# Kernel tuning notes

Measured on AMD Instinct MI355X. Metric: run time of the kernel, lower is better.

## Reference

```python
import jax, jax.numpy as jnp
import numpy as np

B, T = 512, 256
DX, DZ, DH, DDZ, DDX = 1024, 256, 512, 256, 256


def setup_inputs() -> dict:
    key = jax.random.key(0)
    ks = jax.random.split(key, 16)
    s = 0.05
    return {
        "eps": jax.random.normal(ks[0], (B, T, DZ), jnp.float32),
        # stoch_trans dz: h -> relu -> (loc, softplus scale)
        "dz_W1": jax.random.normal(ks[1], (DDZ, DH), jnp.float32) * s,
        "dz_b1": jnp.zeros((DDZ,), jnp.float32),
        "dz_Wloc": jax.random.normal(ks[2], (DZ, DDZ), jnp.float32) * s,
        "dz_bloc": jnp.zeros((DZ,), jnp.float32),
        "dz_Wscale": jax.random.normal(ks[3], (DZ, DDZ), jnp.float32) * s,
        "dz_bscale": jnp.zeros((DZ,), jnp.float32),
        # GRU cell (PyTorch layout: gates [r, z, n] stacked)
        "gru_Wih": jax.random.normal(ks[4], (3 * DH, DZ), jnp.float32) * s,
        "gru_Whh": jax.random.normal(ks[5], (3 * DH, DH), jnp.float32) * s,
        "gru_bih": jnp.zeros((3 * DH,), jnp.float32),
        "gru_bhh": jnp.zeros((3 * DH,), jnp.float32),
        # emitter dx: h -> relu -> sigmoid probs
        "dx_W1": jax.random.normal(ks[6], (DDX, DH), jnp.float32) * s,
        "dx_b1": jnp.zeros((DDX,), jnp.float32),
        "dx_W2": jax.random.normal(ks[7], (DX, DDX), jnp.float32) * s,
        "dx_b2": jnp.zeros((DX,), jnp.float32),
        "h0": jnp.zeros((DH,), jnp.float32),
    }


def reference(eps, dz_W1, dz_b1, dz_Wloc, dz_bloc, dz_Wscale, dz_bscale,
              gru_Wih, gru_Whh, gru_bih, gru_bhh,
              dx_W1, dx_b1, dx_W2, dx_b2, h0):
    batch = eps.shape[0]
    h_init = jnp.broadcast_to(h0[None, :], (batch, h0.shape[0]))

    def step(h, eps_t):
        # stochastic transition: z_loc, z_scale from h_{t-1}
        hid = jax.nn.relu(h @ dz_W1.T + dz_b1)
        z_loc = hid @ dz_Wloc.T + dz_bloc
        z_scale = jax.nn.softplus(hid @ dz_Wscale.T + dz_bscale)
        z_t = z_loc + z_scale * eps_t  # reparameterized Normal sample
        # GRU cell (torch equations)
        gi = z_t @ gru_Wih.T + gru_bih
        gh = h @ gru_Whh.T + gru_bhh
        i_r, i_z, i_n = jnp.split(gi, 3, axis=-1)
        h_r, h_z, h_n = jnp.split(gh, 3, axis=-1)
        r = jax.nn.sigmoid(i_r + h_r)
        u = jax.nn.sigmoid(i_z + h_z)
        n = jnp.tanh(i_n + r * h_n)
        h_new = (1.0 - u) * n + u * h
        # emitter: Bernoulli probs
        hid2 = jax.nn.relu(h_new @ dx_W1.T + dx_b1)
        x_ps = jax.nn.sigmoid(hid2 @ dx_W2.T + dx_b2)
        return h_new, x_ps

    eps_tb = jnp.swapaxes(eps, 0, 1)  # [T, B, DZ]
    _, x_ps = jax.lax.scan(step, h_init, eps_tb)
    return jnp.swapaxes(x_ps, 0, 1)  # [B, T, DX]
```

## Files before the change

kernel.cpp:

```cpp
#include <hip/hip_runtime.h>
#include <hip/hip_bf16.h>

#define DEV __device__ __forceinline__

typedef __bf16 bf16x8 __attribute__((ext_vector_type(8)));
typedef float  f32x4  __attribute__((ext_vector_type(4)));

constexpr int BB  = 512;
constexpr int TT  = 256;
constexpr int DX  = 1024;
constexpr int DZ  = 256;
constexpr int DH  = 512;

DEV f32x4 mfma16(bf16x8 a, bf16x8 b, f32x4 c) {
    return __builtin_amdgcn_mfma_f32_16x16x32_bf16(a, b, c, 0, 0, 0);
}
DEV float sigf(float x) { return 1.0f / (1.0f + __expf(-x)); }
DEV float tanhf_(float x) {
    float e = __expf(-2.0f * fabsf(x));
    float r = (1.0f - e) / (1.0f + e);
    return copysignf(r, x);
}
DEV float softplusf(float x) {
    float m = fmaxf(x, 0.0f);
    return m + __logf(__expf(x - m) + __expf(-m));
}

DEV void st16_wt(void* p, bf16x8 v) {
    asm volatile("global_store_dwordx4 %0, %1, off sc0 sc1" :: "v"(p), "v"(v) : "memory");
}
DEV void st_flag(unsigned* p, unsigned v) {
    asm volatile("global_store_dword %0, %1, off sc0 sc1" :: "v"(p), "v"(v) : "memory");
}
DEV unsigned ld_flag(const unsigned* p) {
    unsigned v;
    asm volatile("global_load_dword %0, %1, off sc0 sc1\n\ts_waitcnt vmcnt(0)"
                 : "=v"(v) : "v"(p) : "memory");
    return v;
}
#define CC_LOAD(dst, p) \
    asm volatile("global_load_dwordx4 %0, %1, off sc0 sc1" : "=v"(dst) : "v"(p))
#define VMCNT0 do { \
    asm volatile("s_waitcnt vmcnt(0)" ::: "memory"); \
    __builtin_amdgcn_sched_barrier(0); } while (0)
#define LGKM0 do { \
    asm volatile("s_waitcnt lgkmcnt(0)" ::: "memory"); \
    __builtin_amdgcn_sched_barrier(0); } while (0)

DEV void wave_wait(const unsigned* base, int nslots, int wv, unsigned tgt) {
    const int lane = threadIdx.x & 63;
    const unsigned* p = base + (((lane & (nslots - 1)) * 4 + wv) * 32);
    while (true) {
        unsigned v = ld_flag(p);
        if (__all((int)(v >= tgt))) break;
    }
}

struct CvtArgs {
    const float* src[7];
    __bf16* dst[7];
    int n[7];
};
__global__ void cvt_weights(CvtArgs a, const float* h0, __bf16* h0buf) {
    int idx = blockIdx.x * blockDim.x + threadIdx.x;
    int stride = gridDim.x * blockDim.x;
    for (int s = 0; s < 7; ++s) {
        const float* sp = a.src[s];
        __bf16* dp = a.dst[s];
        int n = a.n[s];
        for (int i = idx; i < n; i += stride) dp[i] = (__bf16)sp[i];
    }
    for (int i = idx; i < 512 * 512; i += stride) h0buf[i] = (__bf16)h0[i & 511];
}

__global__ __launch_bounds__(256, 1) void phase1c(
    const float* __restrict__ eps,
    const float* __restrict__ b1,  const float* __restrict__ bloc,
    const float* __restrict__ bscale, const float* __restrict__ bih,
    const float* __restrict__ bhh,
    const __bf16* __restrict__ wW1,   const __bf16* __restrict__ wWloc,
    const __bf16* __restrict__ wWscale, const __bf16* __restrict__ wWih,
    const __bf16* __restrict__ wWhh,
    const __bf16* __restrict__ h0buf,
    unsigned* __restrict__ flags,
    char* __restrict__ outb)
{
    __shared__ __bf16 lds[75776];

    const int tid  = threadIdx.x;
    const int w    = tid >> 6;
    const int lane = tid & 63;
    const int r16  = lane & 15;
    const int g4   = lane >> 4;
    const int g    = blockIdx.x & 7;
    const int r    = blockIdx.x >> 3;
    unsigned* gfl   = flags + g * 4096;
    unsigned* flagA = gfl;
    unsigned* flagB = gfl + 2048;
    unsigned* flagC = gfl + 3072;
    const int rowW  = g * 64 + w * 16;

    auto stage = [&](const __bf16* src, __bf16* dst, int R, int C) {
        int chunks = R * C / 8;
        for (int ch = tid; ch < chunks; ch += 256) {
            int row = ch / (C / 8), cc = (ch % (C / 8)) * 8;
            bf16x8 v = *(const bf16x8*)(src + (size_t)row * C + cc);
            *(bf16x8*)(dst + ((row * C + cc) ^ ((row & 7) << 3))) = v;
        }
    };

    if (r < 8) {
        stage(wW1     + (size_t)(r * 32) * 512, lds,         32, 512);
        stage(wWloc   + (size_t)(r * 32) * 256, lds + 16384, 32, 256);
        stage(wWscale + (size_t)(r * 32) * 256, lds + 24576, 32, 256);
        __bf16* wb = lds + 32768 + w * 512;
        const int zc0 = r * 32;
        float bb1[2], bbl[2], bbs[2];
        #pragma unroll
        for (int tt = 0; tt < 2; ++tt) {
            int c = zc0 + tt * 16 + r16;
            bb1[tt] = b1[c]; bbl[tt] = bloc[c]; bbs[tt] = bscale[c];
        }
        __syncthreads();

        for (int t = 0; t < TT; ++t) {
            float ev[2][4];
            #pragma unroll
            for (int tt = 0; tt < 2; ++tt)
                #pragma unroll
                for (int i = 0; i < 4; ++i) {
                    int row = rowW + 4 * g4 + i;
                    ev[tt][i] = __builtin_nontemporal_load(
                        eps + ((size_t)row * TT + t) * DZ + zc0 + tt * 16 + r16);
                }
            if (t) wave_wait(flagA, 16, w, t);
            const char* hp = (t == 0)
                ? (const char*)(h0buf + (size_t)(rowW + r16) * 512) + g4 * 16
                : outb + ((size_t)(rowW + r16) * TT + (t - 1)) * 4096 + 2048 + g4 * 16;
            bf16x8 hv[16];
            #pragma unroll
            for (int kk = 0; kk < 16; ++kk) CC_LOAD(hv[kk], hp + kk * 64);
            VMCNT0;
            f32x4 acc0 = {0,0,0,0}, acc1 = {0,0,0,0};
            #pragma unroll
            for (int kk = 0; kk < 16; ++kk) {
                int l0 = r16, l1 = 16 + r16;
                acc0 = mfma16(hv[kk], *(const bf16x8*)(lds + ((l0 * 512 + kk * 32 + g4 * 8) ^ ((l0 & 7) << 3))), acc0);
                acc1 = mfma16(hv[kk], *(const bf16x8*)(lds + ((l1 * 512 + kk * 32 + g4 * 8) ^ ((l1 & 7) << 3))), acc1);
            }
            #pragma unroll
            for (int tt = 0; tt < 2; ++tt) {
                f32x4 ac = tt ? acc1 : acc0;
                #pragma unroll
                for (int i = 0; i < 4; ++i)
                    wb[(4 * g4 + i) * 32 + tt * 16 + r16] = (__bf16)fmaxf(ac[i] + bb1[tt], 0.0f);
            }
            LGKM0;
            {
                int rl = lane >> 2, ch = lane & 3;
                bf16x8 v = *(const bf16x8*)(wb + rl * 32 + ch * 8);
                st16_wt(outb + ((size_t)(rowW + rl) * TT + t) * 4096 + 3072 + (zc0 + ch * 8) * 2, v);
            }
            VMCNT0;
            if (lane == 0) st_flag(flagB + (r * 4 + w) * 32, t + 1);
            wave_wait(flagB, 8, w, t + 1);
            const char* qp = outb + ((size_t)(rowW + r16) * TT + t) * 4096 + 3072 + g4 * 16;
            bf16x8 qv[8];
            #pragma unroll
            for (int kk = 0; kk < 8; ++kk) CC_LOAD(qv[kk], qp + kk * 64);
            VMCNT0;
            f32x4 aL0 = {0,0,0,0}, aL1 = {0,0,0,0}, aS0 = {0,0,0,0}, aS1 = {0,0,0,0};
            #pragma unroll
            for (int kk = 0; kk < 8; ++kk) {
                int l0 = r16, l1 = 16 + r16;
                int s0 = (l0 * 256 + kk * 32 + g4 * 8) ^ ((l0 & 7) << 3);
                int s1 = (l1 * 256 + kk * 32 + g4 * 8) ^ ((l1 & 7) << 3);
                aL0 = mfma16(qv[kk], *(const bf16x8*)(lds + 16384 + s0), aL0);
                aL1 = mfma16(qv[kk], *(const bf16x8*)(lds + 16384 + s1), aL1);
                aS0 = mfma16(qv[kk], *(const bf16x8*)(lds + 24576 + s0), aS0);
                aS1 = mfma16(qv[kk], *(const bf16x8*)(lds + 24576 + s1), aS1);
            }
            #pragma unroll
            for (int tt = 0; tt < 2; ++tt) {
                f32x4 L = tt ? aL1 : aL0, S = tt ? aS1 : aS0;
                #pragma unroll
                for (int i = 0; i < 4; ++i) {
                    float z = (L[i] + bbl[tt]) + softplusf(S[i] + bbs[tt]) * ev[tt][i];
                    wb[(4 * g4 + i) * 32 + tt * 16 + r16] = (__bf16)z;
                }
            }
            LGKM0;
            {
                int rl = lane >> 2, ch = lane & 3;
                bf16x8 v = *(const bf16x8*)(wb + rl * 32 + ch * 8);
                st16_wt(outb + ((size_t)(rowW + rl) * TT + t) * 4096 + 3584 + (zc0 + ch * 8) * 2, v);
            }
            VMCNT0;
            if (lane == 0) st_flag(flagC + (r * 4 + w) * 32, t + 1);
        }
    } else {
        const int c0 = (r - 8) * 32;
        for (int gg = 0; gg < 3; ++gg) {
            stage(wWhh + (size_t)(512 * gg + c0) * 512, lds + gg * 16384, 32, 512);
            stage(wWih + (size_t)(512 * gg + c0) * 256, lds + 49152 + gg * 8192, 32, 256);
        }
        __bf16* wb = lds + 73728 + w * 512;
        float bI[3][2], bH[3][2];
        #pragma unroll
        for (int gg = 0; gg < 3; ++gg)
            #pragma unroll
            for (int tt = 0; tt < 2; ++tt) {
                int col = 512 * gg + c0 + tt * 16 + r16;
                bI[gg][tt] = bih[col];
                bH[gg][tt] = bhh[col];
            }
        float hreg[2][4];
        #pragma unroll
        for (int tt = 0; tt < 2; ++tt) {
            float v = (float)h0buf[c0 + tt * 16 + r16];
            #pragma unroll
            for (int i = 0; i < 4; ++i) hreg[tt][i] = v;
        }
        __syncthreads();

        for (int t = 0; t < TT; ++t) {
            if (t) wave_wait(flagA, 16, w, t);
            const char* hp = (t == 0)
                ? (const char*)(h0buf + (size_t)(rowW + r16) * 512) + g4 * 16
                : outb + ((size_t)(rowW + r16) * TT + (t - 1)) * 4096 + 2048 + g4 * 16;
            bf16x8 hv[16];
            #pragma unroll
            for (int kk = 0; kk < 16; ++kk) CC_LOAD(hv[kk], hp + kk * 64);
            VMCNT0;
            f32x4 gh[6];
            #pragma unroll
            for (int j = 0; j < 6; ++j) gh[j] = (f32x4){0,0,0,0};
            #pragma unroll
            for (int kk = 0; kk < 16; ++kk) {
                #pragma unroll
                for (int j = 0; j < 6; ++j) {
                    int gg = j >> 1, lr = (j & 1) * 16 + r16;
                    gh[j] = mfma16(hv[kk], *(const bf16x8*)(lds + gg * 16384 +
                              ((lr * 512 + kk * 32 + g4 * 8) ^ ((lr & 7) << 3))), gh[j]);
                }
            }
            wave_wait(flagC, 8, w, t + 1);
            const char* zp = outb + ((size_t)(rowW + r16) * TT + t) * 4096 + 3584 + g4 * 16;
            bf16x8 zv[8];
            #pragma unroll
            for (int kk = 0; kk < 8; ++kk) CC_LOAD(zv[kk], zp + kk * 64);
            VMCNT0;
            f32x4 gi[6];
            #pragma unroll
            for (int j = 0; j < 6; ++j) gi[j] = (f32x4){0,0,0,0};
            #pragma unroll
            for (int kk = 0; kk < 8; ++kk) {
                #pragma unroll
                for (int j = 0; j < 6; ++j) {
                    int gg = j >> 1, lr = (j & 1) * 16 + r16;
                    gi[j] = mfma16(zv[kk], *(const bf16x8*)(lds + 49152 + gg * 8192 +
                              ((lr * 256 + kk * 32 + g4 * 8) ^ ((lr & 7) << 3))), gi[j]);
                }
            }
            #pragma unroll
            for (int tt = 0; tt < 2; ++tt) {
                #pragma unroll
                for (int i = 0; i < 4; ++i) {
                    float rr = sigf(gi[0 + tt][i] + bI[0][tt] + gh[0 + tt][i] + bH[0][tt]);
                    float uu = sigf(gi[2 + tt][i] + bI[1][tt] + gh[2 + tt][i] + bH[1][tt]);
                    float nn = tanhf_(gi[4 + tt][i] + bI[2][tt] + rr * (gh[4 + tt][i] + bH[2][tt]));
                    float hv2 = (1.0f - uu) * nn + uu * hreg[tt][i];
                    hreg[tt][i] = hv2;
                    wb[(4 * g4 + i) * 32 + tt * 16 + r16] = (__bf16)hv2;
                }
            }
            LGKM0;
            {
                int rl = lane >> 2, ch = lane & 3;
                bf16x8 v = *(const bf16x8*)(wb + rl * 32 + ch * 8);
                st16_wt(outb + ((size_t)(rowW + rl) * TT + t) * 4096 + 2048 + (c0 + ch * 8) * 2, v);
            }
            VMCNT0;
            if (lane == 0) st_flag(flagA + ((r - 8) * 4 + w) * 32, t + 1);
        }
    }
}

__global__ __launch_bounds__(256, 3) void phase2(
    const float* __restrict__ db1, const float* __restrict__ db2,
    const __bf16* __restrict__ W1, const __bf16* __restrict__ W2,
    float* __restrict__ out)
{
    __shared__ __bf16 hS  [32 * 512];
    __shared__ __bf16 hid2[32 * 256];

    const int tid  = threadIdx.x;
    const int w    = tid >> 6;
    const int lane = tid & 63;
    const int r16  = lane & 15;
    const int g4   = lane >> 4;
    const size_t row0 = (size_t)blockIdx.x * 32;

    #pragma unroll
    for (int it = 0; it < 8; ++it) {
        int chunk = it * 256 + tid;
        int row = chunk >> 6;
        int cc  = (chunk & 63) * 8;
        bf16x8 v = __builtin_nontemporal_load(
            (const bf16x8*)((const char*)out + (row0 + row) * 4096 + 2048 + cc * 2));
        *(bf16x8*)(hS + ((row * 512 + cc) ^ ((row & 7) << 3))) = v;
    }
    __syncthreads();

    {
        f32x4 acc[2][4];
        #pragma unroll
        for (int rt = 0; rt < 2; ++rt)
            #pragma unroll
            for (int ct = 0; ct < 4; ++ct) acc[rt][ct] = (f32x4){0,0,0,0};
        const __bf16* pB[4];
        #pragma unroll
        for (int ct = 0; ct < 4; ++ct)
            pB[ct] = W1 + (w * 64 + 16 * ct + r16) * 512 + g4 * 8;
        #pragma unroll
        for (int kk = 0; kk < 16; ++kk) {
            bf16x8 a[2];
            #pragma unroll
            for (int rt = 0; rt < 2; ++rt) {
                int row = rt * 16 + r16;
                a[rt] = *(const bf16x8*)(hS + ((row * 512 + kk * 32 + g4 * 8) ^ ((row & 7) << 3)));
            }
            #pragma unroll
            for (int ct = 0; ct < 4; ++ct) {
                bf16x8 b = *(const bf16x8*)(pB[ct] + kk * 32);
                acc[0][ct] = mfma16(a[0], b, acc[0][ct]);
                acc[1][ct] = mfma16(a[1], b, acc[1][ct]);
            }
        }
        #pragma unroll
        for (int ct = 0; ct < 4; ++ct) {
            int col = w * 64 + 16 * ct + r16;
            float bias = db1[col];
            #pragma unroll
            for (int rt = 0; rt < 2; ++rt)
                #pragma unroll
                for (int i = 0; i < 4; ++i) {
                    int row = rt * 16 + g4 * 4 + i;
                    hid2[(row * 256 + col) ^ ((row & 7) << 3)] =
                        (__bf16)fmaxf(acc[rt][ct][i] + bias, 0.0f);
                }
        }
    }
    __syncthreads();

    #pragma unroll
    for (int c = 0; c < 4; ++c) {
        f32x4 acc[2][4];
        #pragma unroll
        for (int rt = 0; rt < 2; ++rt)
            #pragma unroll
            for (int ct = 0; ct < 4; ++ct) acc[rt][ct] = (f32x4){0,0,0,0};
        const __bf16* pB[4];
        #pragma unroll
        for (int ct = 0; ct < 4; ++ct)
            pB[ct] = W2 + (w * 256 + c * 64 + 16 * ct + r16) * 256 + g4 * 8;
        #pragma unroll
        for (int kk = 0; kk < 8; ++kk) {
            bf16x8 a[2];
            #pragma unroll
            for (int rt = 0; rt < 2; ++rt) {
                int row = rt * 16 + r16;
                a[rt] = *(const bf16x8*)(hid2 + ((row * 256 + kk * 32 + g4 * 8) ^ ((row & 7) << 3)));
            }
            #pragma unroll
            for (int ct = 0; ct < 4; ++ct) {
                bf16x8 b = *(const bf16x8*)(pB[ct] + kk * 32);
                acc[0][ct] = mfma16(a[0], b, acc[0][ct]);
                acc[1][ct] = mfma16(a[1], b, acc[1][ct]);
            }
        }
        #pragma unroll
        for (int ct = 0; ct < 4; ++ct) {
            int col = w * 256 + c * 64 + 16 * ct + r16;
            float bias = db2[col];
            #pragma unroll
            for (int rt = 0; rt < 2; ++rt)
                #pragma unroll
                for (int i = 0; i < 4; ++i) {
                    int row = rt * 16 + g4 * 4 + i;
                    __builtin_nontemporal_store(sigf(acc[rt][ct][i] + bias),
                                                out + (row0 + row) * DX + col);
                }
        }
    }
}

extern "C" void kernel_launch(void* const* d_in, const int* in_sizes, int n_in,
                              void* d_out, int out_size, void* d_ws, size_t ws_size,
                              hipStream_t stream) {
    const float* eps       = (const float*)d_in[0];
    const float* dz_W1     = (const float*)d_in[1];
    const float* dz_b1     = (const float*)d_in[2];
    const float* dz_Wloc   = (const float*)d_in[3];
    const float* dz_bloc   = (const float*)d_in[4];
    const float* dz_Wscale = (const float*)d_in[5];
    const float* dz_bscale = (const float*)d_in[6];
    const float* gru_Wih   = (const float*)d_in[7];
    const float* gru_Whh   = (const float*)d_in[8];
    const float* gru_bih   = (const float*)d_in[9];
    const float* gru_bhh   = (const float*)d_in[10];
    const float* dx_W1     = (const float*)d_in[11];
    const float* dx_b1     = (const float*)d_in[12];
    const float* dx_W2     = (const float*)d_in[13];
    const float* dx_b2     = (const float*)d_in[14];
    const float* h0        = (const float*)d_in[15];
    float* out = (float*)d_out;
    char* ws = (char*)d_ws;

    __bf16* wW1     = (__bf16*)(ws + 0);
    __bf16* wWloc   = (__bf16*)(ws + 262144);
    __bf16* wWscale = (__bf16*)(ws + 393216);
    __bf16* wWih    = (__bf16*)(ws + 524288);
    __bf16* wWhh    = (__bf16*)(ws + 1310720);
    __bf16* wdxW1   = (__bf16*)(ws + 2883584);
    __bf16* wdxW2   = (__bf16*)(ws + 3145728);
    __bf16* h0buf   = (__bf16*)(ws + 3670016);
    unsigned* flags = (unsigned*)(ws + 4194304);

    hipMemsetAsync(flags, 0, 131072, stream);

    CvtArgs ca;
    ca.src[0] = dz_W1;     ca.dst[0] = wW1;     ca.n[0] = 256 * 512;
    ca.src[1] = dz_Wloc;   ca.dst[1] = wWloc;   ca.n[1] = 256 * 256;
    ca.src[2] = dz_Wscale; ca.dst[2] = wWscale; ca.n[2] = 256 * 256;
    ca.src[3] = gru_Wih;   ca.dst[3] = wWih;    ca.n[3] = 1536 * 256;
    ca.src[4] = gru_Whh;   ca.dst[4] = wWhh;    ca.n[4] = 1536 * 512;
    ca.src[5] = dx_W1;     ca.dst[5] = wdxW1;   ca.n[5] = 256 * 512;
    ca.src[6] = dx_W2;     ca.dst[6] = wdxW2;   ca.n[6] = 1024 * 256;

    cvt_weights<<<1024, 256, 0, stream>>>(ca, h0, h0buf);
    phase1c<<<192, 256, 0, stream>>>(eps, dz_b1, dz_bloc, dz_bscale,
                                     gru_bih, gru_bhh,
                                     wW1, wWloc, wWscale, wWih, wWhh,
                                     h0buf, flags, (char*)out);
    phase2<<<(BB * TT) / 32, 256, 0, stream>>>(dx_b1, dx_b2, wdxW1, wdxW2, out);
}
```

Before: 2.819 ms.

## Fuse emitter into recurrent kernel using spare blocks that consume h as it is produced

Merges the separate emitter kernel into the persistent recurrence kernel. 64 extra blocks wait on per-step flags and compute the dx MLP and sigmoid outputs while the recurrence runs, so emitter work overlaps the latency-bound scan instead of running afterwards. The flag polling is also restructured to keep two loads in flight and to skip each wave's own slot. This relies on all 256 blocks being co-resident and adds polling traffic that competes with the critical recurrence path.

```diff
diff --git a/kernel.cpp b/kernel.cpp
--- a/kernel.cpp
+++ b/kernel.cpp
@@ -26,20 +26,20 @@
     return m + __logf(__expf(x - m) + __expf(-m));
 }
 
-DEV void st16_wt(void* p, bf16x8 v) {
+DEV void st16_cc(void* p, bf16x8 v) {
     asm volatile("global_store_dwordx4 %0, %1, off sc0 sc1" :: "v"(p), "v"(v) : "memory");
 }
 DEV void st_flag(unsigned* p, unsigned v) {
     asm volatile("global_store_dword %0, %1, off sc0 sc1" :: "v"(p), "v"(v) : "memory");
 }
-DEV unsigned ld_flag(const unsigned* p) {
-    unsigned v;
-    asm volatile("global_load_dword %0, %1, off sc0 sc1\n\ts_waitcnt vmcnt(0)"
-                 : "=v"(v) : "v"(p) : "memory");
-    return v;
-}
-#define CC_LOAD(dst, p) \
-    asm volatile("global_load_dwordx4 %0, %1, off sc0 sc1" : "=v"(dst) : "v"(p))
+#define LDI(dst, p) \
+    asm volatile("global_load_dword %0, %1, off sc0 sc1" : "=v"(dst) : "v"(p) : "memory")
+DEV unsigned wait_older(unsigned vin) {
+    unsigned vout;
+    asm volatile("s_waitcnt vmcnt(1)\n\tv_mov_b32 %0, %1"
+                 : "=v"(vout) : "v"(vin) : "memory");
+    return vout;
+}
 #define VMCNT0 do { \
     asm volatile("s_waitcnt vmcnt(0)" ::: "memory"); \
     __builtin_amdgcn_sched_barrier(0); } while (0)
@@ -47,13 +47,43 @@
     asm volatile("s_waitcnt lgkmcnt(0)" ::: "memory"); \
     __builtin_amdgcn_sched_barrier(0); } while (0)
 
-DEV void wave_wait(const unsigned* base, int nslots, int wv, unsigned tgt) {
+template <int N>
+DEV void loadN(bf16x8* v, const char* p) {
+    #pragma unroll
+    for (int k = 0; k < N; ++k)
+        asm volatile("global_load_dwordx4 %0, %1, off sc0 sc1" : "=v"(v[k]) : "v"(p + k * 64));
+    VMCNT0;
+}
+
+DEV void wave_wait(const unsigned* f, int n, int w, unsigned tgt, int self) {
     const int lane = threadIdx.x & 63;
-    const unsigned* p = base + (((lane & (nslots - 1)) * 4 + wv) * 32);
+    const int slot = lane & (n - 1);
+    const unsigned* p = f + ((slot * 4 + w) * 32);
+    const int skip = (slot == self);
+    VMCNT0;
+    unsigned v0, v1;
+    LDI(v0, p);
     while (true) {
-        unsigned v = ld_flag(p);
-        if (__all((int)(v >= tgt))) break;
+        LDI(v1, p);
+        if (__all(skip | (int)(wait_older(v0) >= tgt))) break;
+        LDI(v0, p);
+        if (__all(skip | (int)(wait_older(v1) >= tgt))) break;
     }
+    VMCNT0;
+}
+DEV void cons_wait(const unsigned* f, unsigned tgt) {
+    const int lane = threadIdx.x & 63;
+    const unsigned* p = f + lane * 32;
+    VMCNT0;
+    unsigned v0, v1;
+    LDI(v0, p);
+    while (true) {
+        LDI(v1, p);
+        if (__all((int)(wait_older(v0) >= tgt))) break;
+        LDI(v0, p);
+        if (__all((int)(wait_older(v1) >= tgt))) break;
+    }
+    VMCNT0;
 }
 
 struct CvtArgs {
@@ -73,7 +103,7 @@
     for (int i = idx; i < 512 * 512; i += stride) h0buf[i] = (__bf16)h0[i & 511];
 }
 
-__global__ __launch_bounds__(256, 1) void phase1c(
+__global__ __launch_bounds__(256, 1) void fused(
     const float* __restrict__ eps,
     const float* __restrict__ b1,  const float* __restrict__ bloc,
     const float* __restrict__ bscale, const float* __restrict__ bih,
@@ -81,6 +111,8 @@
     const __bf16* __restrict__ wW1,   const __bf16* __restrict__ wWloc,
     const __bf16* __restrict__ wWscale, const __bf16* __restrict__ wWih,
     const __bf16* __restrict__ wWhh,
+    const float* __restrict__ db1, const float* __restrict__ db2,
+    const __bf16* __restrict__ dxW1, const __bf16* __restrict__ dxW2,
     const __bf16* __restrict__ h0buf,
     unsigned* __restrict__ flags,
     char* __restrict__ outb)
@@ -92,305 +124,312 @@
     const int lane = tid & 63;
     const int r16  = lane & 15;
     const int g4   = lane >> 4;
-    const int g    = blockIdx.x & 7;
-    const int r    = blockIdx.x >> 3;
-    unsigned* gfl   = flags + g * 4096;
-    unsigned* flagA = gfl;
-    unsigned* flagB = gfl + 2048;
-    unsigned* flagC = gfl + 3072;
-    const int rowW  = g * 64 + w * 16;
-
-    auto stage = [&](const __bf16* src, __bf16* dst, int R, int C) {
-        int chunks = R * C / 8;
-        for (int ch = tid; ch < chunks; ch += 256) {
-            int row = ch / (C / 8), cc = (ch % (C / 8)) * 8;
-            bf16x8 v = *(const bf16x8*)(src + (size_t)row * C + cc);
-            *(bf16x8*)(dst + ((row * C + cc) ^ ((row & 7) << 3))) = v;
-        }
-    };
-
-    if (r < 8) {
-        stage(wW1     + (size_t)(r * 32) * 512, lds,         32, 512);
-        stage(wWloc   + (size_t)(r * 32) * 256, lds + 16384, 32, 256);
-        stage(wWscale + (size_t)(r * 32) * 256, lds + 24576, 32, 256);
-        __bf16* wb = lds + 32768 + w * 512;
-        const int zc0 = r * 32;
-        float bb1[2], bbl[2], bbs[2];
-        #pragma unroll
-        for (int tt = 0; tt < 2; ++tt) {
-            int c = zc0 + tt * 16 + r16;
-            bb1[tt] = b1[c]; bbl[tt] = bloc[c]; bbs[tt] = bscale[c];
-        }
-        __syncthreads();
-
-        for (int t = 0; t < TT; ++t) {
-            float ev[2][4];
-            #pragma unroll
-            for (int tt = 0; tt < 2; ++tt)
-                #pragma unroll
-                for (int i = 0; i < 4; ++i) {
-                    int row = rowW + 4 * g4 + i;
-                    ev[tt][i] = __builtin_nontemporal_load(
-                        eps + ((size_t)row * TT + t) * DZ + zc0 + tt * 16 + r16);
-                }
-            if (t) wave_wait(flagA, 16, w, t);
-            const char* hp = (t == 0)
-                ? (const char*)(h0buf + (size_t)(rowW + r16) * 512) + g4 * 16
-                : outb + ((size_t)(rowW + r16) * TT + (t - 1)) * 4096 + 2048 + g4 * 16;
-            bf16x8 hv[16];
-            #pragma unroll
-            for (int kk = 0; kk < 16; ++kk) CC_LOAD(hv[kk], hp + kk * 64);
-            VMCNT0;
-            f32x4 acc0 = {0,0,0,0}, acc1 = {0,0,0,0};
-            #pragma unroll
-            for (int kk = 0; kk < 16; ++kk) {
-                int l0 = r16, l1 = 16 + r16;
-                acc0 = mfma16(hv[kk], *(const bf16x8*)(lds + ((l0 * 512 + kk * 32 + g4 * 8) ^ ((l0 & 7) << 3))), acc0);
-                acc1 = mfma16(hv[kk], *(const bf16x8*)(lds + ((l1 * 512 + kk * 32 + g4 * 8) ^ ((l1 & 7) << 3))), acc1);
-            }
+
+    if (blockIdx.x < 192) {
+        const int g = blockIdx.x & 7;
+        const int r = blockIdx.x >> 3;
+        unsigned* gfl   = flags + g * 4096;
+        unsigned* flagA = gfl;
+        unsigned* flagB = gfl + 2048;
+        unsigned* flagC = gfl + 3072;
+        const int rowW  = g * 64 + w * 16;
+
+        auto stage = [&](const __bf16* src, __bf16* dst, int R, int C) {
+            int chunks = R * C / 8;
+            for (int ch = tid; ch < chunks; ch += 256) {
+                int row = ch / (C / 8), cc = (ch % (C / 8)) * 8;
+                bf16x8 v = *(const bf16x8*)(src + (size_t)row * C + cc);
+                *(bf16x8*)(dst + ((row * C + cc) ^ ((row & 7) << 3))) = v;
+            }
+        };
+
+        if (r < 8) {
+            stage(wW1     + (size_t)(r * 32) * 512, lds,         32, 512);
+            stage(wWloc   + (size_t)(r * 32) * 256, lds + 16384, 32, 256);
+            stage(wWscale + (size_t)(r * 32) * 256, lds + 24576, 32, 256);
+            __bf16* wb = lds + 32768 + w * 512;
+            const int zc0 = r * 32;
+            float bb1[2], bbl[2], bbs[2];
             #pragma unroll
             for (int tt = 0; tt < 2; ++tt) {
-                f32x4 ac = tt ? acc1 : acc0;
-                #pragma unroll
-                for (int i = 0; i < 4; ++i)
-                    wb[(4 * g4 + i) * 32 + tt * 16 + r16] = (__bf16)fmaxf(ac[i] + bb1[tt], 0.0f);
-            }
-            LGKM0;
-            {
-                int rl = lane >> 2, ch = lane & 3;
-                bf16x8 v = *(const bf16x8*)(wb + rl * 32 + ch * 8);
-                st16_wt(outb + ((size_t)(rowW + rl) * TT + t) * 4096 + 3072 + (zc0 + ch * 8) * 2, v);
-            }
-            VMCNT0;
-            if (lane == 0) st_flag(flagB + (r * 4 + w) * 32, t + 1);
-            wave_wait(flagB, 8, w, t + 1);
-            const char* qp = outb + ((size_t)(rowW + r16) * TT + t) * 4096 + 3072 + g4 * 16;
-            bf16x8 qv[8];
+                int c = zc0 + tt * 16 + r16;
+                bb1[tt] = b1[c]; bbl[tt] = bloc[c]; bbs[tt] = bscale[c];
+            }
+            __syncthreads();
+
+            for (int t = 0; t < TT; ++t) {
+                float ev[2][4];
+                #pragma unroll
+                for (int tt = 0; tt < 2; ++tt)
+                    #pragma unroll
+                    for (int i = 0; i < 4; ++i) {
+                        int row = rowW + 4 * g4 + i;
+                        ev[tt][i] = __builtin_nontemporal_load(
+                            eps + ((size_t)row * TT + t) * DZ + zc0 + tt * 16 + r16);
+                    }
+                if (t) wave_wait(flagA, 16, w, t, -1);
+                const char* hp = (t == 0)
+                    ? (const char*)(h0buf + (size_t)(rowW + r16) * 512) + g4 * 16
+                    : outb + ((size_t)(rowW + r16) * TT + (t - 1)) * 4096 + 2048 + g4 * 16;
+                bf16x8 hv[16];
+                loadN<16>(hv, hp);
+                f32x4 acc0 = {0,0,0,0}, acc1 = {0,0,0,0};
+                #pragma unroll
+                for (int kk = 0; kk < 16; ++kk) {
+                    int l0 = r16, l1 = 16 + r16;
+                    acc0 = mfma16(hv[kk], *(const bf16x8*)(lds + ((l0 * 512 + kk * 32 + g4 * 8) ^ ((l0 & 7) << 3))), acc0);
+                    acc1 = mfma16(hv[kk], *(const bf16x8*)(lds + ((l1 * 512 + kk * 32 + g4 * 8) ^ ((l1 & 7) << 3))), acc1);
+                }
+                #pragma unroll
+                for (int tt = 0; tt < 2; ++tt) {
+                    f32x4 ac = tt ? acc1 : acc0;
+                    #pragma unroll
+                    for (int i = 0; i < 4; ++i)
+                        wb[(4 * g4 + i) * 32 + tt * 16 + r16] = (__bf16)fmaxf(ac[i] + bb1[tt], 0.0f);
+                }
+                LGKM0;
+                {
+                    int rl = lane >> 2, ch = lane & 3;
+                    bf16x8 v = *(const bf16x8*)(wb + rl * 32 + ch * 8);
+                    st16_cc(outb + ((size_t)(rowW + rl) * TT + t) * 4096 + 3072 + (zc0 + ch * 8) * 2, v);
+                }
+                VMCNT0;
+                if (lane == 0) st_flag(flagB + (r * 4 + w) * 32, t + 1);
+                wave_wait(flagB, 8, w, t + 1, r);
+                const char* qp = outb + ((size_t)(rowW + r16) * TT + t) * 4096 + 3072 + g4 * 16;
+                bf16x8 qv[8];
+                loadN<8>(qv, qp);
+                f32x4 aL0 = {0,0,0,0}, aL1 = {0,0,0,0}, aS0 = {0,0,0,0}, aS1 = {0,0,0,0};
+                #pragma unroll
+                for (int kk = 0; kk < 8; ++kk) {
+                    int l0 = r16, l1 = 16 + r16;
+                    int s0 = (l0 * 256 + kk * 32 + g4 * 8) ^ ((l0 & 7) << 3);
+                    int s1 = (l1 * 256 + kk * 32 + g4 * 8) ^ ((l1 & 7) << 3);
+                    aL0 = mfma16(qv[kk], *(const bf16x8*)(lds + 16384 + s0), aL0);
+                    aL1 = mfma16(qv[kk], *(const bf16x8*)(lds + 16384 + s1), aL1);
+                    aS0 = mfma16(qv[kk], *(const bf16x8*)(lds + 24576 + s0), aS0);
+                    aS1 = mfma16(qv[kk], *(const bf16x8*)(lds + 24576 + s1), aS1);
+                }
+                #pragma unroll
+                for (int tt = 0; tt < 2; ++tt) {
+                    f32x4 L = tt ? aL1 : aL0, S = tt ? aS1 : aS0;
+                    #pragma unroll
+                    for (int i = 0; i < 4; ++i) {
+                        float z = (L[i] + bbl[tt]) + softplusf(S[i] + bbs[tt]) * ev[tt][i];
+                        wb[(4 * g4 + i) * 32 + tt * 16 + r16] = (__bf16)z;
+                    }
+                }
+                LGKM0;
+                {
+                    int rl = lane >> 2, ch = lane & 3;
+                    bf16x8 v = *(const bf16x8*)(wb + rl * 32 + ch * 8);
+                    st16_cc(outb + ((size_t)(rowW + rl) * TT + t) * 4096 + 3584 + (zc0 + ch * 8) * 2, v);
+                }
+                VMCNT0;
+                if (lane == 0) st_flag(flagC + (r * 4 + w) * 32, t + 1);
+            }
+        } else {
+            const int c0 = (r - 8) * 32;
+            for (int gg = 0; gg < 3; ++gg) {
+                stage(wWhh + (size_t)(512 * gg + c0) * 512, lds + gg * 16384, 32, 512);
+                stage(wWih + (size_t)(512 * gg + c0) * 256, lds + 49152 + gg * 8192, 32, 256);
+            }
+            __bf16* wb = lds + 73728 + w * 512;
+            float bI[3][2], bH[3][2];
             #pragma unroll
-            for (int kk = 0; kk < 8; ++kk) CC_LOAD(qv[kk], qp + kk * 64);
-            VMCNT0;
-            f32x4 aL0 = {0,0,0,0}, aL1 = {0,0,0,0}, aS0 = {0,0,0,0}, aS1 = {0,0,0,0};
-            #pragma unroll
-            for (int kk = 0; kk < 8; ++kk) {
-                int l0 = r16, l1 = 16 + r16;
-                int s0 = (l0 * 256 + kk * 32 + g4 * 8) ^ ((l0 & 7) << 3);
-                int s1 = (l1 * 256 + kk * 32 + g4 * 8) ^ ((l1 & 7) << 3);
-                aL0 = mfma16(qv[kk], *(const bf16x8*)(lds + 16384 + s0), aL0);
-                aL1 = mfma16(qv[kk], *(const bf16x8*)(lds + 16384 + s1), aL1);
-                aS0 = mfma16(qv[kk], *(const bf16x8*)(lds + 24576 + s0), aS0);
-                aS1 = mfma16(qv[kk], *(const bf16x8*)(lds + 24576 + s1), aS1);
-            }
+            for (int gg = 0; gg < 3; ++gg)
+                #pragma unroll
+                for (int tt = 0; tt < 2; ++tt) {
+                    int col = 512 * gg + c0 + tt * 16 + r16;
+                    bI[gg][tt] = bih[col];
+                    bH[gg][tt] = bhh[col];
+                }
+            float hreg[2][4];
             #pragma unroll
             for (int tt = 0; tt < 2; ++tt) {
-                f32x4 L = tt ? aL1 : aL0, S = tt ? aS1 : aS0;
-                #pragma unroll
-                for (int i = 0; i < 4; ++i) {
-                    float z = (L[i] + bbl[tt]) + softplusf(S[i] + bbs[tt]) * ev[tt][i];
-                    wb[(4 * g4 + i) * 32 + tt * 16 + r16] = (__bf16)z;
-                }
-            }
-            LGKM0;
-            {
-                int rl = lane >> 2, ch = lane & 3;
-                bf16x8 v = *(const bf16x8*)(wb + rl * 32 + ch * 8);
-                st16_wt(outb + ((size_t)(rowW + rl) * TT + t) * 4096 + 3584 + (zc0 + ch * 8) * 2, v);
-            }
-            VMCNT0;
-            if (lane == 0) st_flag(flagC + (r * 4 + w) * 32, t + 1);
+                float v = (float)h0buf[c0 + tt * 16 + r16];
+                #pragma unroll
+                for (int i = 0; i < 4; ++i) hreg[tt][i] = v;
+            }
+            __syncthreads();
+
+            for (int t = 0; t < TT; ++t) {
+                if (t) wave_wait(flagA, 16, w, t, r - 8);
+                const char* hp = (t == 0)
+                    ? (const char*)(h0buf + (size_t)(rowW + r16) * 512) + g4 * 16
+                    : outb + ((size_t)(rowW + r16) * TT + (t - 1)) * 4096 + 2048 + g4 * 16;
+                bf16x8 hv[16];
+                loadN<16>(hv, hp);
+                f32x4 gh[6];
+                #pragma unroll
+                for (int j = 0; j < 6; ++j) gh[j] = (f32x4){0,0,0,0};
+                #pragma unroll
+                for (int kk = 0; kk < 16; ++kk) {
+                    #pragma unroll
+                    for (int j = 0; j < 6; ++j) {
+                        int gg = j >> 1, lr = (j & 1) * 16 + r16;
+                        gh[j] = mfma16(hv[kk], *(const bf16x8*)(lds + gg * 16384 +
+                                  ((lr * 512 + kk * 32 + g4 * 8) ^ ((lr & 7) << 3))), gh[j]);
+                    }
+                }
+                wave_wait(flagC, 8, w, t + 1, -1);
+                const char* zp = outb + ((size_t)(rowW + r16) * TT + t) * 4096 + 3584 + g4 * 16;
+                bf16x8 zv[8];
+                loadN<8>(zv, zp);
+                f32x4 gi[6];
+                #pragma unroll
+                for (int j = 0; j < 6; ++j) gi[j] = (f32x4){0,0,0,0};
+                #pragma unroll
+                for (int kk = 0; kk < 8; ++kk) {
+                    #pragma unroll
+                    for (int j = 0; j < 6; ++j) {
+                        int gg = j >> 1, lr = (j & 1) * 16 + r16;
+                        gi[j] = mfma16(zv[kk], *(const bf16x8*)(lds + 49152 + gg * 8192 +
+                                  ((lr * 256 + kk * 32 + g4 * 8) ^ ((lr & 7) << 3))), gi[j]);
+                    }
+                }
+                #pragma unroll
+                for (int tt = 0; tt < 2; ++tt) {
+                    #pragma unroll
+                    for (int i = 0; i < 4; ++i) {
+                        float rr = sigf(gi[0 + tt][i] + bI[0][tt] + gh[0 + tt][i] + bH[0][tt]);
+                        float uu = sigf(gi[2 + tt][i] + bI[1][tt] + gh[2 + tt][i] + bH[1][tt]);
+                        float nn = tanhf_(gi[4 + tt][i] + bI[2][tt] + rr * (gh[4 + tt][i] + bH[2][tt]));
+                        float hv2 = (1.0f - uu) * nn + uu * hreg[tt][i];
+                        hreg[tt][i] = hv2;
+                        wb[(4 * g4 + i) * 32 + tt * 16 + r16] = (__bf16)hv2;
+                    }
+                }
+                LGKM0;
+                {
+                    int rl = lane >> 2, ch = lane & 3;
+                    bf16x8 v = *(const bf16x8*)(wb + rl * 32 + ch * 8);
+                    st16_cc(outb + ((size_t)(rowW + rl) * TT + t) * 4096 + 2048 + (c0 + ch * 8) * 2, v);
+                }
+                VMCNT0;
+                if (lane == 0) st_flag(flagA + ((r - 8) * 4 + w) * 32, t + 1);
+            }
         }
     } else {
-        const int c0 = (r - 8) * 32;
-        for (int gg = 0; gg < 3; ++gg) {
-            stage(wWhh + (size_t)(512 * gg + c0) * 512, lds + gg * 16384, 32, 512);
-            stage(wWih + (size_t)(512 * gg + c0) * 256, lds + 49152 + gg * 8192, 32, 256);
-        }
-        __bf16* wb = lds + 73728 + w * 512;
-        float bI[3][2], bH[3][2];
-        #pragma unroll
-        for (int gg = 0; gg < 3; ++gg)
+        const int c   = blockIdx.x - 192;
+        const int g   = c & 7;
+        const int ph  = c >> 3;
+        unsigned* flagA = flags + g * 4096;
+        __bf16* hS   = lds;
+        __bf16* hid2 = lds + 32768;
+        const int rowB = g * 64;
+
+        for (int t = ph; t < TT; t += 8) {
+            unsigned tgt = (t + 2 <= TT) ? (unsigned)(t + 2) : (unsigned)TT;
+            if (tid < 64) cons_wait(flagA, tgt);
+            __syncthreads();
+
+            {
+                bf16x8 v[8];
+                #pragma unroll
+                for (int half = 0; half < 2; ++half) {
+                    #pragma unroll
+                    for (int it = 0; it < 8; ++it) {
+                        int chunk = (half * 8 + it) * 256 + tid;
+                        int row = chunk >> 6, cc = (chunk & 63) * 8;
+                        const char* p = outb + ((size_t)(rowB + row) * TT + t) * 4096 + 2048 + cc * 2;
+                        asm volatile("global_load_dwordx4 %0, %1, off sc0 sc1" : "=v"(v[it]) : "v"(p));
+                    }
+                    VMCNT0;
+                    #pragma unroll
+                    for (int it = 0; it < 8; ++it) {
+                        int chunk = (half * 8 + it) * 256 + tid;
+                        int row = chunk >> 6, cc = (chunk & 63) * 8;
+                        *(bf16x8*)(hS + ((row * 512 + cc) ^ ((row & 7) << 3))) = v[it];
+                    }
+                }
+            }
+            __syncthreads();
+
+            {
+                f32x4 acc[4][4];
+                #pragma unroll
+                for (int rt = 0; rt < 4; ++rt)
+                    #pragma unroll
+                    for (int ct = 0; ct < 4; ++ct) acc[rt][ct] = (f32x4){0,0,0,0};
+                const __bf16* pB[4];
+                #pragma unroll
+                for (int ct = 0; ct < 4; ++ct)
+                    pB[ct] = dxW1 + (w * 64 + 16 * ct + r16) * 512 + g4 * 8;
+                #pragma unroll
+                for (int kk = 0; kk < 16; ++kk) {
+                    bf16x8 a[4];
+                    #pragma unroll
+                    for (int rt = 0; rt < 4; ++rt) {
+                        int row = rt * 16 + r16;
+                        a[rt] = *(const bf16x8*)(hS + ((row * 512 + kk * 32 + g4 * 8) ^ ((row & 7) << 3)));
+                    }
+                    #pragma unroll
+                    for (int ct = 0; ct < 4; ++ct) {
+                        bf16x8 b = *(const bf16x8*)(pB[ct] + kk * 32);
+                        #pragma unroll
+                        for (int rt = 0; rt < 4; ++rt)
+                            acc[rt][ct] = mfma16(a[rt], b, acc[rt][ct]);
+                    }
+                }
+                #pragma unroll
+                for (int ct = 0; ct < 4; ++ct) {
+                    int col = w * 64 + 16 * ct + r16;
+                    float bias = db1[col];
+                    #pragma unroll
+                    for (int rt = 0; rt < 4; ++rt)
+                        #pragma unroll
+                        for (int i = 0; i < 4; ++i) {
+                            int row = rt * 16 + g4 * 4 + i;
+                            hid2[(row * 256 + col) ^ ((row & 7) << 3)] =
+                                (__bf16)fmaxf(acc[rt][ct][i] + bias, 0.0f);
+                        }
+                }
+            }
+            __syncthreads();
+
             #pragma unroll
-            for (int tt = 0; tt < 2; ++tt) {
-                int col = 512 * gg + c0 + tt * 16 + r16;
-                bI[gg][tt] = bih[col];
-                bH[gg][tt] = bhh[col];
-            }
-        float hreg[2][4];
-        #pragma unroll
-        for (int tt = 0; tt < 2; ++tt) {
-            float v = (float)h0buf[c0 + tt * 16 + r16];
-            #pragma unroll
-            for (int i = 0; i < 4; ++i) hreg[tt][i] = v;
-        }
-        __syncthreads();
-
-        for (int t = 0; t < TT; ++t) {
-            if (t) wave_wait(flagA, 16, w, t);
-            const char* hp = (t == 0)
-                ? (const char*)(h0buf + (size_t)(rowW + r16) * 512) + g4 * 16
-                : outb + ((size_t)(rowW + r16) * TT + (t - 1)) * 4096 + 2048 + g4 * 16;
-            bf16x8 hv[16];
-            #pragma unroll
-            for (int kk = 0; kk < 16; ++kk) CC_LOAD(hv[kk], hp + kk * 64);
-            VMCNT0;
-            f32x4 gh[6];
-            #pragma unroll
-            for (int j = 0; j < 6; ++j) gh[j] = (f32x4){0,0,0,0};
-            #pragma unroll
-            for (int kk = 0; kk < 16; ++kk) {
-                #pragma unroll
-                for (int j = 0; j < 6; ++j) {
-                    int gg = j >> 1, lr = (j & 1) * 16 + r16;
-                    gh[j] = mfma16(hv[kk], *(const bf16x8*)(lds + gg * 16384 +
-                              ((lr * 512 + kk * 32 + g4 * 8) ^ ((lr & 7) << 3))), gh[j]);
-                }
-            }
-            wave_wait(flagC, 8, w, t + 1);
-            const char* zp = outb + ((size_t)(rowW + r16) * TT + t) * 4096 + 3584 + g4 * 16;
-            bf16x8 zv[8];
-            #pragma unroll
-            for (int kk = 0; kk < 8; ++kk) CC_LOAD(zv[kk], zp + kk * 64);
-            VMCNT0;
-            f32x4 gi[6];
-            #pragma unroll
-            for (int j = 0; j < 6; ++j) gi[j] = (f32x4){0,0,0,0};
-            #pragma unroll
-            for (int kk = 0; kk < 8; ++kk) {
-                #pragma unroll
-                for (int j = 0; j < 6; ++j) {
-                    int gg = j >> 1, lr = (j & 1) * 16 + r16;
-                    gi[j] = mfma16(zv[kk], *(const bf16x8*)(lds + 49152 + gg * 8192 +
-                              ((lr * 256 + kk * 32 + g4 * 8) ^ ((lr & 7) << 3))), gi[j]);
-                }
-            }
-            #pragma unroll
-            for (int tt = 0; tt < 2; ++tt) {
-                #pragma unroll
-                for (int i = 0; i < 4; ++i) {
-                    float rr = sigf(gi[0 + tt][i] + bI[0][tt] + gh[0 + tt][i] + bH[0][tt]);
-                    float uu = sigf(gi[2 + tt][i] + bI[1][tt] + gh[2 + tt][i] + bH[1][tt]);
-                    float nn = tanhf_(gi[4 + tt][i] + bI[2][tt] + rr * (gh[4 + tt][i] + bH[2][tt]));
-                    float hv2 = (1.0f - uu) * nn + uu * hreg[tt][i];
-                    hreg[tt][i] = hv2;
-                    wb[(4 * g4 + i) * 32 + tt * 16 + r16] = (__bf16)hv2;
-                }
-            }
-            LGKM0;
-            {
-                int rl = lane >> 2, ch = lane & 3;
-                bf16x8 v = *(const bf16x8*)(wb + rl * 32 + ch * 8);
-                st16_wt(outb + ((size_t)(rowW + rl) * TT + t) * 4096 + 2048 + (c0 + ch * 8) * 2, v);
-            }
-            VMCNT0;
-            if (lane == 0) st_flag(flagA + ((r - 8) * 4 + w) * 32, t + 1);
-        }
-    }
-}
-
-__global__ __launch_bounds__(256, 3) void phase2(
-    const float* __restrict__ db1, const float* __restrict__ db2,
-    const __bf16* __restrict__ W1, const __bf16* __restrict__ W2,
-    float* __restrict__ out)
-{
-    __shared__ __bf16 hS  [32 * 512];
-    __shared__ __bf16 hid2[32 * 256];
-
-    const int tid  = threadIdx.x;
-    const int w    = tid >> 6;
-    const int lane = tid & 63;
-    const int r16  = lane & 15;
-    const int g4   = lane >> 4;
-    const size_t row0 = (size_t)blockIdx.x * 32;
-
-    #pragma unroll
-    for (int it = 0; it < 8; ++it) {
-        int chunk = it * 256 + tid;
-        int row = chunk >> 6;
-        int cc  = (chunk & 63) * 8;
-        bf16x8 v = __builtin_nontemporal_load(
-            (const bf16x8*)((const char*)out + (row0 + row) * 4096 + 2048 + cc * 2));
-        *(bf16x8*)(hS + ((row * 512 + cc) ^ ((row & 7) << 3))) = v;
-    }
-    __syncthreads();
-
-    {
-        f32x4 acc[2][4];
-        #pragma unroll
-        for (int rt = 0; rt < 2; ++rt)
-            #pragma unroll
-            for (int ct = 0; ct < 4; ++ct) acc[rt][ct] = (f32x4){0,0,0,0};
-        const __bf16* pB[4];
-        #pragma unroll
-        for (int ct = 0; ct < 4; ++ct)
-            pB[ct] = W1 + (w * 64 + 16 * ct + r16) * 512 + g4 * 8;
-        #pragma unroll
-        for (int kk = 0; kk < 16; ++kk) {
-            bf16x8 a[2];
-            #pragma unroll
-            for (int rt = 0; rt < 2; ++rt) {
-                int row = rt * 16 + r16;
-                a[rt] = *(const bf16x8*)(hS + ((row * 512 + kk * 32 + g4 * 8) ^ ((row & 7) << 3)));
-            }
-            #pragma unroll
-            for (int ct = 0; ct < 4; ++ct) {
-                bf16x8 b = *(const bf16x8*)(pB[ct] + kk * 32);
-                acc[0][ct] = mfma16(a[0], b, acc[0][ct]);
-                acc[1][ct] = mfma16(a[1], b, acc[1][ct]);
-            }
-        }
-        #pragma unroll
-        for (int ct = 0; ct < 4; ++ct) {
-            int col = w * 64 + 16 * ct + r16;
-            float bias = db1[col];
-            #pragma unroll
-            for (int rt = 0; rt < 2; ++rt)
-                #pragma unroll
-                for (int i = 0; i < 4; ++i) {
-                    int row = rt * 16 + g4 * 4 + i;
-                    hid2[(row * 256 + col) ^ ((row & 7) << 3)] =
-                        (__bf16)fmaxf(acc[rt][ct][i] + bias, 0.0f);
-                }
-        }
-    }
-    __syncthreads();
-
-    #pragma unroll
-    for (int c = 0; c < 4; ++c) {
-        f32x4 acc[2][4];
-        #pragma unroll
-        for (int rt = 0; rt < 2; ++rt)
-            #pragma unroll
-            for (int ct = 0; ct < 4; ++ct) acc[rt][ct] = (f32x4){0,0,0,0};
-        const __bf16* pB[4];
-        #pragma unroll
-        for (int ct = 0; ct < 4; ++ct)
-            pB[ct] = W2 + (w * 256 + c * 64 + 16 * ct + r16) * 256 + g4 * 8;
-        #pragma unroll
-        for (int kk = 0; kk < 8; ++kk) {
-            bf16x8 a[2];
-            #pragma unroll
-            for (int rt = 0; rt < 2; ++rt) {
-                int row = rt * 16 + r16;
-                a[rt] = *(const bf16x8*)(hid2 + ((row * 256 + kk * 32 + g4 * 8) ^ ((row & 7) << 3)));
-            }
-            #pragma unroll
-            for (int ct = 0; ct < 4; ++ct) {
-                bf16x8 b = *(const bf16x8*)(pB[ct] + kk * 32);
-                acc[0][ct] = mfma16(a[0], b, acc[0][ct]);
-                acc[1][ct] = mfma16(a[1], b, acc[1][ct]);
-            }
-        }
-        #pragma unroll
-        for (int ct = 0; ct < 4; ++ct) {
-            int col = w * 256 + c * 64 + 16 * ct + r16;
-            float bias = db2[col];
-            #pragma unroll
-            for (int rt = 0; rt < 2; ++rt)
-                #pragma unroll
-                for (int i = 0; i < 4; ++i) {
-                    int row = rt * 16 + g4 * 4 + i;
-                    __builtin_nontemporal_store(sigf(acc[rt][ct][i] + bias),
-                                                out + (row0 + row) * DX + col);
-                }
+            for (int q = 0; q < 4; ++q) {
+                f32x4 acc[4][4];
+                #pragma unroll
+                for (int rt = 0; rt < 4; ++rt)
+                    #pragma unroll
+                    for (int ct = 0; ct < 4; ++ct) acc[rt][ct] = (f32x4){0,0,0,0};
+                const __bf16* pB[4];
+                #pragma unroll
+                for (int ct = 0; ct < 4; ++ct)
+                    pB[ct] = dxW2 + (w * 256 + q * 64 + 16 * ct + r16) * 256 + g4 * 8;
+                #pragma unroll
+                for (int kk = 0; kk < 8; ++kk) {
+                    bf16x8 a[4];
+                    #pragma unroll
+                    for (int rt = 0; rt < 4; ++rt) {
+                        int row = rt * 16 + r16;
+                        a[rt] = *(const bf16x8*)(hid2 + ((row * 256 + kk * 32 + g4 * 8) ^ ((row & 7) << 3)));
+                    }
+                    #pragma unroll
+                    for (int ct = 0; ct < 4; ++ct) {
+                        bf16x8 b = *(const bf16x8*)(pB[ct] + kk * 32);
+                        #pragma unroll
+                        for (int rt = 0; rt < 4; ++rt)
+                            acc[rt][ct] = mfma16(a[rt], b, acc[rt][ct]);
+                    }
+                }
+                #pragma unroll
+                for (int ct = 0; ct < 4; ++ct) {
+                    int col = w * 256 + q * 64 + 16 * ct + r16;
+                    float bias = db2[col];
+                    #pragma unroll
+                    for (int rt = 0; rt < 4; ++rt)
+                        #pragma unroll
+                        for (int i = 0; i < 4; ++i) {
+                            int row = rt * 16 + g4 * 4 + i;
+                            float* dst = (float*)(outb + ((size_t)(rowB + row) * TT + t) * 4096) + col;
+                            __builtin_nontemporal_store(sigf(acc[rt][ct][i] + bias), dst);
+                        }
+                }
+            }
+            __syncthreads();
         }
     }
 }
@@ -439,9 +478,9 @@
     ca.src[6] = dx_W2;     ca.dst[6] = wdxW2;   ca.n[6] = 1024 * 256;
 
     cvt_weights<<<1024, 256, 0, stream>>>(ca, h0, h0buf);
-    phase1c<<<192, 256, 0, stream>>>(eps, dz_b1, dz_bloc, dz_bscale,
-                                     gru_bih, gru_bhh,
-                                     wW1, wWloc, wWscale, wWih, wWhh,
-                                     h0buf, flags, (char*)out);
-    phase2<<<(BB * TT) / 32, 256, 0, stream>>>(dx_b1, dx_b2, wdxW1, wdxW2, out);
-}
+    fused<<<256, 256, 0, stream>>>(eps, dz_b1, dz_bloc, dz_bscale,
+                                   gru_bih, gru_bhh,
+                                   wW1, wWloc, wWscale, wWih, wWhh,
+                                   dx_b1, dx_b2, wdxW1, wdxW2,
+                                   h0buf, flags, (char*)out);
+}
```

Result: faster. 2.592 ms (-8.1%).
